# Kernel optimization log

Measured on AMD Instinct MI355X. Metric: run time of the kernel, lower is better.

Reference implementation:

```python
import jax, jax.numpy as jnp
import numpy as np

A_BITS = 7   # activation - 1, per T_quantize(norm(x), activation-1)
W_BITS = 7   # weight quantization levels bits (IRlinear, bit=weight)
HEADS = 16
DIM_HEAD = 64
LN_EPS = 1e-5


def qfn(x, bit):
    """Symmetric per-tensor uniform quantization with straight-through estimator.
    bit >= 31 means bypass (fp path, matching weight/activation == 32 defaults)."""
    if bit >= 31:
        return x
    n = jnp.asarray(2.0 ** bit - 1.0, x.dtype)
    s = jnp.max(jnp.abs(x))
    s = jnp.where(s == 0, jnp.asarray(1.0, x.dtype), s)
    y = jnp.round(x / s * n) / n * s
    # STE: forward uses quantized value, gradient passes through unchanged
    return x + jax.lax.stop_gradient(y - x)


def setup_inputs() -> dict:
    key = jax.random.key(0)
    kx, kq, ko = jax.random.split(key, 3)
    B, N, C = 8, 1024, 1024
    inner = HEADS * DIM_HEAD  # 1024
    x = jax.random.normal(kx, (B, N, C), dtype=jnp.float32)
    gamma = jnp.ones((C,), dtype=jnp.float32)
    beta = jnp.zeros((C,), dtype=jnp.float32)
    W_qkv = jax.random.normal(kq, (3 * inner, C), dtype=jnp.float32) * 0.02
    W_out = jax.random.normal(ko, (C, inner), dtype=jnp.float32) * 0.02
    b_out = jnp.zeros((C,), dtype=jnp.float32)
    return {"x": x, "gamma": gamma, "beta": beta,
            "W_qkv": W_qkv, "W_out": W_out, "b_out": b_out}


def reference(x, gamma, beta, W_qkv, W_out, b_out):
    B, N, C = x.shape
    H, Dh = HEADS, DIM_HEAD
    # LayerNorm
    mu = jnp.mean(x, axis=-1, keepdims=True)
    var = jnp.mean(jnp.square(x - mu), axis=-1, keepdims=True)
    xn = (x - mu) * jax.lax.rsqrt(var + LN_EPS) * gamma + beta
    # activation quantization (T_quantize with activation-1 bits)
    xq = qfn(xn, A_BITS)
    # quantized QKV projection (IRlinear, no bias)
    qkv = jnp.einsum('bnc,oc->bno', xq, qfn(W_qkv, W_BITS))
    qkv = qkv.reshape(B, N, 3, H, Dh).transpose(2, 0, 3, 1, 4)  # [3,B,H,N,Dh]
    q, k, v = qkv[0], qkv[1], qkv[2]
    # scaled dot-product attention (dropout_p = 0)
    scale = Dh ** -0.5
    scores = jnp.einsum('bhqd,bhkd->bhqk', q, k) * scale
    attn = jax.nn.softmax(scores, axis=-1)
    o = jnp.einsum('bhqk,bhkd->bhqd', attn, v)  # [B,H,N,Dh]
    o = o.transpose(0, 2, 1, 3).reshape(B, N, H * Dh)
    # quantized output projection (IRlinear, with bias)
    out = jnp.einsum('bni,ci->bnc', o, qfn(W_out, W_BITS)) + b_out
    return out
```

## Files before the change

### kernel.cpp

```cpp
#include <hip/hip_runtime.h>
#include <hip/hip_bf16.h>
#include <math.h>

typedef unsigned int u32;
typedef unsigned short u16;
using f32x4  = __attribute__((ext_vector_type(4))) float;
using f32x16 = __attribute__((ext_vector_type(16))) float;
using bfrag  = __attribute__((ext_vector_type(8))) short;
using i32x4  = __attribute__((ext_vector_type(4))) int;
union FragU { uint4 u; bfrag f; };
union FragI { uint4 u; i32x4 f; };

#define HEADS 16
#define DH    64
#define NB    8
#define NN    1024
#define NC    1024
#define M_TOT 8192
#define O_QKV 3072
#define KDIM  1024
#define LOG2E 1.44269504088896340736f

static __device__ __forceinline__ u16 f2bf(float f) {
  u32 u = __float_as_uint(f);
  return (u16)((u + 0x7fffu + ((u >> 16) & 1u)) >> 16);
}
static __device__ __forceinline__ float bf2f(u16 h) { return __uint_as_float(((u32)h) << 16); }
static __device__ __forceinline__ u32 pk_bf16(float a, float b) {
  __hip_bfloat162 h = __float22bfloat162_rn(make_float2(a, b));
  u32 r; __builtin_memcpy(&r, &h, 4); return r;
}

static __device__ __forceinline__ float wave_sum(float v) {
#pragma unroll
  for (int off = 32; off > 0; off >>= 1) v += __shfl_xor(v, off, 64);
  return v;
}
static __device__ __forceinline__ float wave_max(float v) {
#pragma unroll
  for (int off = 32; off > 0; off >>= 1) v = fmaxf(v, __shfl_xor(v, off, 64));
  return v;
}

static __device__ __forceinline__ f32x4 mfma16(FragU a, FragU b, f32x4 c) {
  return __builtin_amdgcn_mfma_f32_16x16x32_bf16(a.f, b.f, c, 0, 0, 0);
}
static __device__ __forceinline__ f32x16 mfma32(FragU a, FragU b, f32x16 c) {
  return __builtin_amdgcn_mfma_f32_32x32x16_bf16(a.f, b.f, c, 0, 0, 0);
}
static __device__ __forceinline__ i32x4 mfma16i(FragI a, FragI b, i32x4 c) {
  return __builtin_amdgcn_mfma_i32_16x16x64_i8(a.f, b.f, c, 0, 0, 0);
}

static __device__ __forceinline__ void pl32swap(u32& a, u32& b) {
#if __has_builtin(__builtin_amdgcn_permlane32_swap)
  using u32x2 = __attribute__((ext_vector_type(2))) unsigned int;
  u32x2 r = __builtin_amdgcn_permlane32_swap(a, b, false, false);
  a = r[0]; b = r[1];
#else
  asm volatile("v_permlane32_swap_b32 %0, %1" : "+v"(a), "+v"(b));
#endif
}

template<int P, int BLK>
static __device__ __forceinline__ void stage_rows(const char* g, int row_stride,
                                                  char* ldsb, int t) {
#pragma unroll
  for (int p = 0; p < P; ++p) {
    const int c = p * BLK + t;
    const int row = c >> 3, kc = c & 7;
    const char* gp = g + (size_t)row * row_stride + ((kc ^ (row & 7)) << 4);
    char* lp = ldsb + ((p * BLK + (t & ~63)) << 4);
    __builtin_amdgcn_global_load_lds((const __attribute__((address_space(1))) void*)gp,
                                     (__attribute__((address_space(3))) void*)lp, 16, 0, 0);
  }
}
static __device__ __forceinline__ uint4 ld_chunk(const char* base, int row, int chunk) {
  return *(const uint4*)(base + (((row << 3) + (chunk ^ (row & 7))) << 4));
}

__global__ __launch_bounds__(256) void absmax2_kernel(const float4* __restrict__ wq,
    const float4* __restrict__ wo, float* __restrict__ wqp, float* __restrict__ wop) {
  const float4* p; int n4, bid, nb; float* o;
  if (blockIdx.x < 512) { p = wq; n4 = O_QKV * KDIM / 4; o = wqp + blockIdx.x; bid = blockIdx.x; nb = 512; }
  else                  { p = wo; n4 = NC * KDIM / 4;    o = wop + blockIdx.x - 512; bid = blockIdx.x - 512; nb = 256; }
  float m = 0.f;
  for (int i = bid * 256 + threadIdx.x; i < n4; i += nb * 256) {
    float4 v = p[i];
    m = fmaxf(m, fmaxf(fmaxf(fabsf(v.x), fabsf(v.y)), fmaxf(fabsf(v.z), fabsf(v.w))));
  }
  m = wave_max(m);
  __shared__ float red[4];
  if ((threadIdx.x & 63) == 0) red[threadIdx.x >> 6] = m;
  __syncthreads();
  if (threadIdx.x == 0) *o = fmaxf(fmaxf(red[0], red[1]), fmaxf(red[2], red[3]));
}

__global__ __launch_bounds__(256) void ln_pass(const float* __restrict__ x,
    const float* __restrict__ g, const float* __restrict__ b,
    float2* __restrict__ mrs, float* __restrict__ actp)
{
  const int t = threadIdx.x, w = t >> 6, l = t & 63;
  const int row = (blockIdx.x << 2) + w;
  const float4* xr = (const float4*)(x + (size_t)row * NC);
  float4 v[4];
#pragma unroll
  for (int j = 0; j < 4; ++j) v[j] = xr[l + (j << 6)];

  float s = 0.f;
#pragma unroll
  for (int j = 0; j < 4; ++j) s += (v[j].x + v[j].y) + (v[j].z + v[j].w);
  s = wave_sum(s);
  const float mu = s * (1.0f / NC);

  float ss = 0.f;
#pragma unroll
  for (int j = 0; j < 4; ++j) {
    const float dx = v[j].x - mu, dy = v[j].y - mu, dz = v[j].z - mu, dw = v[j].w - mu;
    ss += (dx * dx + dy * dy) + (dz * dz + dw * dw);
  }
  ss = wave_sum(ss);
  const float rstd = 1.0f / sqrtf(ss * (1.0f / NC) + 1e-5f);
  if (l == 0) mrs[row] = make_float2(mu, rstd);

  float am = 0.f;
#pragma unroll
  for (int j = 0; j < 4; ++j) {
    const float4 gv = ((const float4*)g)[l + (j << 6)];
    const float4 bv = ((const float4*)b)[l + (j << 6)];
    const float yx = (v[j].x - mu) * rstd * gv.x + bv.x;
    const float yy = (v[j].y - mu) * rstd * gv.y + bv.y;
    const float yz = (v[j].z - mu) * rstd * gv.z + bv.z;
    const float yw = (v[j].w - mu) * rstd * gv.w + bv.w;
    am = fmaxf(am, fmaxf(fmaxf(fabsf(yx), fabsf(yy)), fmaxf(fabsf(yz), fabsf(yw))));
  }
  am = wave_max(am);
  __shared__ float red[4];
  if (l == 0) red[w] = am;
  __syncthreads();
  if (t == 0) actp[blockIdx.x] = fmaxf(fmaxf(red[0], red[1]), fmaxf(red[2], red[3]));
}

__global__ __launch_bounds__(256) void reduce3(const float* __restrict__ actp,
    const float* __restrict__ wqp, const float* __restrict__ wop,
    unsigned* __restrict__ scal)
{
  const int t = threadIdx.x;
  float a = 0.f, q = 0.f, o = 0.f;
#pragma unroll
  for (int k = 0; k < 8; ++k) a = fmaxf(a, actp[t + (k << 8)]);
  a = fmaxf(a, 0.f);
  q = fmaxf(wqp[t], wqp[t + 256]);
  o = wop[t];
  a = wave_max(a); q = wave_max(q); o = wave_max(o);
  __shared__ float ra[4], rq[4], ro[4];
  if ((t & 63) == 0) { ra[t >> 6] = a; rq[t >> 6] = q; ro[t >> 6] = o; }
  __syncthreads();
  if (t == 0) {
    a = fmaxf(fmaxf(ra[0], ra[1]), fmaxf(ra[2], ra[3]));
    q = fmaxf(fmaxf(rq[0], rq[1]), fmaxf(rq[2], rq[3]));
    o = fmaxf(fmaxf(ro[0], ro[1]), fmaxf(ro[2], ro[3]));
    scal[0] = __float_as_uint(a == 0.f ? 1.f : a);
    scal[1] = __float_as_uint(q == 0.f ? 1.f : q);
    scal[2] = __float_as_uint(o == 0.f ? 1.f : o);
  }
}

__global__ __launch_bounds__(256) void quant_x_kernel(const float* __restrict__ x,
    const float* __restrict__ g, const float* __restrict__ b,
    const float2* __restrict__ mrs, const unsigned* __restrict__ sb,
    u32* __restrict__ xq)
{
  const int t = threadIdx.x;
  const long long row = blockIdx.x;
  const float2 ms = mrs[row];
  const float s = __uint_as_float(*sb);
  const float4 v = ((const float4*)(x + row * NC))[t];
  const float4 gv = ((const float4*)g)[t];
  const float4 bv = ((const float4*)b)[t];
  float4 y;
  y.x = (v.x - ms.x) * ms.y * gv.x + bv.x;
  y.y = (v.y - ms.x) * ms.y * gv.y + bv.y;
  y.z = (v.z - ms.x) * ms.y * gv.z + bv.z;
  y.w = (v.w - ms.x) * ms.y * gv.w + bv.w;
  const int ia = (int)rintf(y.x / s * 127.0f);
  const int ib = (int)rintf(y.y / s * 127.0f);
  const int ic = (int)rintf(y.z / s * 127.0f);
  const int id = (int)rintf(y.w / s * 127.0f);
  xq[row * 256 + t] = (u32)(ia & 255) | ((u32)(ib & 255) << 8)
                    | ((u32)(ic & 255) << 16) | ((u32)(id & 255) << 24);
}

__global__ __launch_bounds__(256) void quant_w_kernel(const float4* __restrict__ wq,
    u32* __restrict__ oq, const float4* __restrict__ wo, uint2* __restrict__ oo,
    const unsigned* __restrict__ scal) {
  if (blockIdx.x < 768) {
    const float s = __uint_as_float(scal[1]);
    const int base = blockIdx.x << 10;
#pragma unroll
    for (int k = 0; k < 4; ++k) {
      const int i = base + (k << 8) + threadIdx.x;
      float4 v = wq[i];
      const int ia = (int)rintf(v.x / s * 127.0f);
      const int ib = (int)rintf(v.y / s * 127.0f);
      const int ic = (int)rintf(v.z / s * 127.0f);
      const int id = (int)rintf(v.w / s * 127.0f);
      oq[i] = (u32)(ia & 255) | ((u32)(ib & 255) << 8)
            | ((u32)(ic & 255) << 16) | ((u32)(id & 255) << 24);
    }
  } else {
    const float s = __uint_as_float(scal[2]);
    const int base = (blockIdx.x - 768) << 10;
#pragma unroll
    for (int k = 0; k < 4; ++k) {
      const int i = base + (k << 8) + threadIdx.x;
      float4 v = wo[i];
      uint2 o;
      o.x = pk_bf16(rintf(v.x / s * 127.0f), rintf(v.y / s * 127.0f));
      o.y = pk_bf16(rintf(v.z / s * 127.0f), rintf(v.w / s * 127.0f));
      oo[i] = o;
    }
  }
}

__global__ __launch_bounds__(256) void gemm_qkv_mfma(const char* __restrict__ A,
    const char* __restrict__ B, const unsigned* __restrict__ scal,
    u16* __restrict__ qp, u16* __restrict__ kp, u16* __restrict__ vtp)
{
  __shared__ __align__(16) char lds[32768];
  char* As = lds;
  char* Bs = lds + 16384;
  const int t = threadIdx.x, w = t >> 6, l = t & 63;
  const int lg = l >> 4, lc = l & 15;
  const int wm = (w >> 1) << 6, wn = (w & 1) << 6;
  i32x4 acc[4][4];
#pragma unroll
  for (int i = 0; i < 4; ++i)
#pragma unroll
    for (int j = 0; j < 4; ++j) acc[i][j] = 0;

  const char* gA = A + ((size_t)blockIdx.y << 7) * KDIM;
  const char* gB = B + ((size_t)blockIdx.x << 7) * KDIM;

  for (int k0 = 0; k0 < KDIM; k0 += 128) {
    stage_rows<4, 256>(gA + k0, KDIM, As, t);
    stage_rows<4, 256>(gB + k0, KDIM, Bs, t);
    __syncthreads();
#pragma unroll
    for (int ks = 0; ks < 2; ++ks) {
      FragI a[4], b[4];
#pragma unroll
      for (int mf = 0; mf < 4; ++mf) a[mf].u = ld_chunk(As, wm + (mf << 4) + lc, (ks << 2) + lg);
#pragma unroll
      for (int nf = 0; nf < 4; ++nf) b[nf].u = ld_chunk(Bs, wn + (nf << 4) + lc, (ks << 2) + lg);
      __builtin_amdgcn_s_setprio(1);
#pragma unroll
      for (int mf = 0; mf < 4; ++mf)
#pragma unroll
        for (int nf = 0; nf < 4; ++nf) acc[mf][nf] = mfma16i(a[mf], b[nf], acc[mf][nf]);
      __builtin_amdgcn_s_setprio(0);
    }
    __syncthreads();
  }

  const float sa = __uint_as_float(scal[0]), sw = __uint_as_float(scal[1]);
  const int which = blockIdx.x >> 3;
  float sc = sa * sw / 16129.0f;
  if (which == 0) sc *= 0.125f * LOG2E;
  const int obase = ((blockIdx.x & 7) << 7) + wn;
  const int mbase = ((int)blockIdx.y << 7) + wm;

  if (which < 2) {
    u16* d_ = which ? kp : qp;
#pragma unroll
    for (int nf = 0; nf < 4; ++nf) {
      const int od = obase + (nf << 4) + lc;
      const int hh = od >> 6, dd = od & 63;
#pragma unroll
      for (int mf = 0; mf < 4; ++mf)
#pragma unroll
        for (int r = 0; r < 4; ++r) {
          const int tok = mbase + (mf << 4) + (lg << 2) + r;
          const size_t addr = ((size_t)((tok >> 10) * HEADS + hh) << 16)
                            + ((size_t)(tok & 1023) << 6) + dd;
          d_[addr] = f2bf((float)acc[mf][nf][r] * sc);
        }
    }
  } else {
#pragma unroll
    for (int nf = 0; nf < 4; ++nf) {
      const int od = obase + (nf << 4) + lc;
      const int hh = od >> 6, dd = od & 63;
#pragma unroll
      for (int mf = 0; mf < 4; ++mf) {
        const int tok0 = mbase + (mf << 4) + (lg << 2);
        uint2 hv;
        hv.x = pk_bf16((float)acc[mf][nf][0] * sc, (float)acc[mf][nf][1] * sc);
        hv.y = pk_bf16((float)acc[mf][nf][2] * sc, (float)acc[mf][nf][3] * sc);
        const size_t base = ((size_t)((tok0 >> 10) * HEADS + hh) << 16)
                          + ((size_t)dd << 10) + (tok0 & 1023);
        *(uint2*)(vtp + base) = hv;
      }
    }
  }
}

__global__ __launch_bounds__(512) void attn_mfma(
    const u16* __restrict__ qp, const u16* __restrict__ kp, const u16* __restrict__ vtp,
    u16* __restrict__ ohp)
{
  __shared__ __align__(16) char lds[32768];
  const int t = threadIdx.x, w = t >> 6, l = t & 63;
  const int l31 = l & 31, h = l >> 5;
  const int id = blockIdx.x;
  const int bh = ((id & 7) << 4) + ((id >> 3) & 15);
  const int qbase = ((id >> 7) << 8) + (w << 5);
  const size_t bhoff = (size_t)bh << 16;

  FragU qf[4];
#pragma unroll
  for (int ks = 0; ks < 4; ++ks)
    qf[ks].u = *(const uint4*)(qp + bhoff + ((size_t)(qbase + l31) << 6) + (ks << 4) + (h << 3));

  f32x16 oacc[2];
  oacc[0] = 0.f; oacc[1] = 0.f;
  float lpart = 0.f;

  stage_rows<1, 512>((const char*)(kp + bhoff), 128, lds, t);
  stage_rows<1, 512>((const char*)(vtp + bhoff), 2048, lds + 8192, t);
  __syncthreads();

  for (int kb = 0; kb < 16; ++kb) {
    char* cur = lds + ((kb & 1) << 14);
    if (kb < 15) {
      char* nxt = lds + (((kb + 1) & 1) << 14);
      const size_t kn = kb + 1;
      stage_rows<1, 512>((const char*)(kp + bhoff + (kn << 12)), 128, nxt, t);
      stage_rows<1, 512>((const char*)(vtp + bhoff + (kn << 6)), 2048, nxt + 8192, t);
    }

    f32x16 s0 = 0.f, s1 = 0.f;
#pragma unroll
    for (int ks = 0; ks < 4; ++ks) {
      FragU k0, k1;
      k0.u = ld_chunk(cur, l31,      (ks << 1) + h);
      k1.u = ld_chunk(cur, 32 + l31, (ks << 1) + h);
      __builtin_amdgcn_s_setprio(1);
      s0 = mfma32(k0, qf[ks], s0);
      s1 = mfma32(k1, qf[ks], s1);
      __builtin_amdgcn_s_setprio(0);
    }

    u32 W0[8], W1[8];
    float lsum = 0.f;
#pragma unroll
    for (int j = 0; j < 8; ++j) {
      const float a0 = __builtin_amdgcn_exp2f(s0[2 * j]);
      const float b0 = __builtin_amdgcn_exp2f(s0[2 * j + 1]);
      const float a1 = __builtin_amdgcn_exp2f(s1[2 * j]);
      const float b1 = __builtin_amdgcn_exp2f(s1[2 * j + 1]);
      lsum += (a0 + b0) + (a1 + b1);
      W0[j] = pk_bf16(a0, b0);
      W1[j] = pk_bf16(a1, b1);
    }
    lpart += lsum;

    FragU pf[4];
#pragma unroll
    for (int kk = 0; kk < 2; ++kk) {
      u32 a0 = W0[4 * kk + 0], b0 = W0[4 * kk + 2];
      u32 a1 = W0[4 * kk + 1], b1 = W0[4 * kk + 3];
      pl32swap(a0, b0); pl32swap(a1, b1);
      pf[kk].u     = make_uint4(a0, a1, b0, b1);
      u32 c0 = W1[4 * kk + 0], d0 = W1[4 * kk + 2];
      u32 c1 = W1[4 * kk + 1], d1 = W1[4 * kk + 3];
      pl32swap(c0, d0); pl32swap(c1, d1);
      pf[2 + kk].u = make_uint4(c0, c1, d0, d1);
    }

#pragma unroll
    for (int ks = 0; ks < 4; ++ks) {
      FragU v0, v1;
      v0.u = ld_chunk(cur + 8192, l31,      (ks << 1) + h);
      v1.u = ld_chunk(cur + 8192, 32 + l31, (ks << 1) + h);
      __builtin_amdgcn_s_setprio(1);
      oacc[0] = mfma32(v0, pf[ks], oacc[0]);
      oacc[1] = mfma32(v1, pf[ks], oacc[1]);
      __builtin_amdgcn_s_setprio(0);
    }
    __syncthreads();
  }

  lpart += __shfl_xor(lpart, 32, 64);
  const float invl = 1.0f / lpart;

  const int b = bh >> 4, hd_ = bh & 15;
  const size_t orow = (size_t)b * NN + qbase + l31;
  u16* ohb = ohp + (orow << 10) + (hd_ << 6);
#pragma unroll
  for (int dt = 0; dt < 2; ++dt)
#pragma unroll
    for (int rg = 0; rg < 4; ++rg) {
      const int d0 = (dt << 5) + (rg << 3) + (h << 2);
      const float v0 = oacc[dt][4 * rg + 0] * invl, v1 = oacc[dt][4 * rg + 1] * invl;
      const float v2 = oacc[dt][4 * rg + 2] * invl, v3 = oacc[dt][4 * rg + 3] * invl;
      uint2 hv;
      hv.x = (u32)f2bf(v0) | ((u32)f2bf(v1) << 16);
      hv.y = (u32)f2bf(v2) | ((u32)f2bf(v3) << 16);
      *(uint2*)(ohb + d0) = hv;
    }
}

__global__ __launch_bounds__(256) void gemm_out_mfma(const u16* __restrict__ Ah,
    const u16* __restrict__ B, const unsigned* __restrict__ scal,
    const float* __restrict__ bias, float* __restrict__ out)
{
  __shared__ __align__(16) char lds[32768];
  char* Ahs = lds;
  char* Bs  = lds + 16384;
  const int t = threadIdx.x, w = t >> 6, l = t & 63;
  const int lg = l >> 4, lc = l & 15;
  const int wm = (w >> 1) << 6, wn = (w & 1) << 6;
  f32x4 acc[4][4];
#pragma unroll
  for (int i = 0; i < 4; ++i)
#pragma unroll
    for (int j = 0; j < 4; ++j) acc[i][j] = 0.f;

  const char* gAh = (const char*)Ah + ((size_t)blockIdx.y << 7) * 2048;
  const char* gB  = (const char*)B  + ((size_t)blockIdx.x << 7) * 2048;

  for (int k0 = 0; k0 < KDIM; k0 += 64) {
    stage_rows<4, 256>(gAh + k0 * 2, 2048, Ahs, t);
    stage_rows<4, 256>(gB  + k0 * 2, 2048, Bs,  t);
    __syncthreads();
#pragma unroll
    for (int ks = 0; ks < 2; ++ks) {
      FragU a[4], b[4];
#pragma unroll
      for (int mf = 0; mf < 4; ++mf) a[mf].u = ld_chunk(Ahs, wm + (mf << 4) + lc, (ks << 2) + lg);
#pragma unroll
      for (int nf = 0; nf < 4; ++nf) b[nf].u = ld_chunk(Bs, wn + (nf << 4) + lc, (ks << 2) + lg);
      __builtin_amdgcn_s_setprio(1);
#pragma unroll
      for (int mf = 0; mf < 4; ++mf)
#pragma unroll
        for (int nf = 0; nf < 4; ++nf) acc[mf][nf] = mfma16(a[mf], b[nf], acc[mf][nf]);
      __builtin_amdgcn_s_setprio(0);
    }
    __syncthreads();
  }

  const float sc = __uint_as_float(scal[2]) / 127.0f;
  const int cb = ((int)blockIdx.x << 7) + wn;
  const int mb = ((int)blockIdx.y << 7) + wm;
#pragma unroll
  for (int nf = 0; nf < 4; ++nf) {
    const int col = cb + (nf << 4) + lc;
    const float bv = bias[col];
#pragma unroll
    for (int mf = 0; mf < 4; ++mf)
#pragma unroll
      for (int r = 0; r < 4; ++r) {
        const int row = mb + (mf << 4) + (lg << 2) + r;
        out[(size_t)row * NC + col] = acc[mf][nf][r] * sc + bv;
      }
  }
}

__global__ void ws_fail_kernel(float* out) { out[0] = 1.0e6f; }

extern "C" void kernel_launch(void* const* d_in, const int* in_sizes, int n_in,
                              void* d_out, int out_size, void* d_ws, size_t ws_size,
                              hipStream_t stream) {
  const float* x     = (const float*)d_in[0];
  const float* gamma = (const float*)d_in[1];
  const float* beta  = (const float*)d_in[2];
  const float* Wqkv  = (const float*)d_in[3];
  const float* Wout  = (const float*)d_in[4];
  const float* bout  = (const float*)d_in[5];
  float* out = (float*)d_out;

  char* ws = (char*)d_ws;
  unsigned* scal = (unsigned*)ws;
  size_t off = 256;
  float* actp = (float*)(ws + off); off += 2048 * 4;
  float* wqp  = (float*)(ws + off); off += 512 * 4;
  float* wop  = (float*)(ws + off); off += 256 * 4;
  off = (off + 255) & ~(size_t)255;
  float2* mrs = (float2*)(ws + off); off += (size_t)M_TOT * 8;
  char* xq  = ws + off; off += (size_t)M_TOT * KDIM;
  char* wqi = ws + off; off += (size_t)O_QKV * KDIM;
  u16* woi = (u16*)(ws + off); off += (size_t)NC * KDIM * 2;
  u16* qb  = (u16*)(ws + off); off += 16777216;
  u16* kb  = (u16*)(ws + off); off += 16777216;
  u16* vtb = (u16*)(ws + off); off += 16777216;
  u16* oh  = (u16*)(ws + off); off += 16777216;
  if (ws_size < off) { ws_fail_kernel<<<1, 1, 0, stream>>>(out); return; }

  absmax2_kernel<<<768, 256, 0, stream>>>((const float4*)Wqkv, (const float4*)Wout, wqp, wop);
  ln_pass<<<2048, 256, 0, stream>>>(x, gamma, beta, mrs, actp);
  reduce3<<<1, 256, 0, stream>>>(actp, wqp, wop, scal);

  quant_x_kernel<<<M_TOT, 256, 0, stream>>>(x, gamma, beta, mrs, scal + 0, (u32*)xq);
  quant_w_kernel<<<1024, 256, 0, stream>>>((const float4*)Wqkv, (u32*)wqi,
                                           (const float4*)Wout, (uint2*)woi, scal);

  dim3 g1(O_QKV / 128, M_TOT / 128);
  gemm_qkv_mfma<<<g1, 256, 0, stream>>>(xq, wqi, scal, qb, kb, vtb);

  attn_mfma<<<512, 512, 0, stream>>>(qb, kb, vtb, oh);

  dim3 g3(NC / 128, M_TOT / 128);
  gemm_out_mfma<<<g3, 256, 0, stream>>>(oh, woi, scal, bout, out);
}
```

Before: 144.7 us.

## Merge prep kernels and double attention key block to 128

Result: faster. 139.2 us, median of 2 (-3.8%).

```diff
diff --git a/kernel.cpp b/kernel.cpp
--- a/kernel.cpp
+++ b/kernel.cpp
@@ -25,7 +25,6 @@
   u32 u = __float_as_uint(f);
   return (u16)((u + 0x7fffu + ((u >> 16) & 1u)) >> 16);
 }
-static __device__ __forceinline__ float bf2f(u16 h) { return __uint_as_float(((u32)h) << 16); }
 static __device__ __forceinline__ u32 pk_bf16(float a, float b) {
   __hip_bfloat162 h = __float22bfloat162_rn(make_float2(a, b));
   u32 r; __builtin_memcpy(&r, &h, 4); return r;
@@ -79,66 +78,64 @@
   return *(const uint4*)(base + (((row << 3) + (chunk ^ (row & 7))) << 4));
 }
 
-__global__ __launch_bounds__(256) void absmax2_kernel(const float4* __restrict__ wq,
-    const float4* __restrict__ wo, float* __restrict__ wqp, float* __restrict__ wop) {
-  const float4* p; int n4, bid, nb; float* o;
-  if (blockIdx.x < 512) { p = wq; n4 = O_QKV * KDIM / 4; o = wqp + blockIdx.x; bid = blockIdx.x; nb = 512; }
-  else                  { p = wo; n4 = NC * KDIM / 4;    o = wop + blockIdx.x - 512; bid = blockIdx.x - 512; nb = 256; }
-  float m = 0.f;
-  for (int i = bid * 256 + threadIdx.x; i < n4; i += nb * 256) {
-    float4 v = p[i];
-    m = fmaxf(m, fmaxf(fmaxf(fabsf(v.x), fabsf(v.y)), fmaxf(fabsf(v.z), fabsf(v.w))));
-  }
-  m = wave_max(m);
+__global__ __launch_bounds__(256) void prep_kernel(const float* __restrict__ x,
+    const float* __restrict__ g, const float* __restrict__ b,
+    const float4* __restrict__ wq, const float4* __restrict__ wo,
+    float2* __restrict__ mrs, float* __restrict__ actp,
+    float* __restrict__ wqp, float* __restrict__ wop)
+{
   __shared__ float red[4];
-  if ((threadIdx.x & 63) == 0) red[threadIdx.x >> 6] = m;
-  __syncthreads();
-  if (threadIdx.x == 0) *o = fmaxf(fmaxf(red[0], red[1]), fmaxf(red[2], red[3]));
-}
-
-__global__ __launch_bounds__(256) void ln_pass(const float* __restrict__ x,
-    const float* __restrict__ g, const float* __restrict__ b,
-    float2* __restrict__ mrs, float* __restrict__ actp)
-{
-  const int t = threadIdx.x, w = t >> 6, l = t & 63;
-  const int row = (blockIdx.x << 2) + w;
-  const float4* xr = (const float4*)(x + (size_t)row * NC);
-  float4 v[4];
-#pragma unroll
-  for (int j = 0; j < 4; ++j) v[j] = xr[l + (j << 6)];
-
-  float s = 0.f;
-#pragma unroll
-  for (int j = 0; j < 4; ++j) s += (v[j].x + v[j].y) + (v[j].z + v[j].w);
-  s = wave_sum(s);
-  const float mu = s * (1.0f / NC);
-
-  float ss = 0.f;
-#pragma unroll
-  for (int j = 0; j < 4; ++j) {
-    const float dx = v[j].x - mu, dy = v[j].y - mu, dz = v[j].z - mu, dw = v[j].w - mu;
-    ss += (dx * dx + dy * dy) + (dz * dz + dw * dw);
-  }
-  ss = wave_sum(ss);
-  const float rstd = 1.0f / sqrtf(ss * (1.0f / NC) + 1e-5f);
-  if (l == 0) mrs[row] = make_float2(mu, rstd);
-
-  float am = 0.f;
-#pragma unroll
-  for (int j = 0; j < 4; ++j) {
-    const float4 gv = ((const float4*)g)[l + (j << 6)];
-    const float4 bv = ((const float4*)b)[l + (j << 6)];
-    const float yx = (v[j].x - mu) * rstd * gv.x + bv.x;
-    const float yy = (v[j].y - mu) * rstd * gv.y + bv.y;
-    const float yz = (v[j].z - mu) * rstd * gv.z + bv.z;
-    const float yw = (v[j].w - mu) * rstd * gv.w + bv.w;
-    am = fmaxf(am, fmaxf(fmaxf(fabsf(yx), fabsf(yy)), fmaxf(fabsf(yz), fabsf(yw))));
-  }
-  am = wave_max(am);
-  __shared__ float red[4];
-  if (l == 0) red[w] = am;
-  __syncthreads();
-  if (t == 0) actp[blockIdx.x] = fmaxf(fmaxf(red[0], red[1]), fmaxf(red[2], red[3]));
+  const int bid = blockIdx.x, t = threadIdx.x;
+  if (bid < 2048) {
+    const int w = t >> 6, l = t & 63;
+    const int row = (bid << 2) + w;
+    const float4* xr = (const float4*)(x + (size_t)row * NC);
+    float4 v[4];
+#pragma unroll
+    for (int j = 0; j < 4; ++j) v[j] = xr[l + (j << 6)];
+    float s = 0.f;
+#pragma unroll
+    for (int j = 0; j < 4; ++j) s += (v[j].x + v[j].y) + (v[j].z + v[j].w);
+    s = wave_sum(s);
+    const float mu = s * (1.0f / NC);
+    float ss = 0.f;
+#pragma unroll
+    for (int j = 0; j < 4; ++j) {
+      const float dx = v[j].x - mu, dy = v[j].y - mu, dz = v[j].z - mu, dw = v[j].w - mu;
+      ss += (dx * dx + dy * dy) + (dz * dz + dw * dw);
+    }
+    ss = wave_sum(ss);
+    const float rstd = 1.0f / sqrtf(ss * (1.0f / NC) + 1e-5f);
+    if (l == 0) mrs[row] = make_float2(mu, rstd);
+    float am = 0.f;
+#pragma unroll
+    for (int j = 0; j < 4; ++j) {
+      const float4 gv = ((const float4*)g)[l + (j << 6)];
+      const float4 bv = ((const float4*)b)[l + (j << 6)];
+      const float yx = (v[j].x - mu) * rstd * gv.x + bv.x;
+      const float yy = (v[j].y - mu) * rstd * gv.y + bv.y;
+      const float yz = (v[j].z - mu) * rstd * gv.z + bv.z;
+      const float yw = (v[j].w - mu) * rstd * gv.w + bv.w;
+      am = fmaxf(am, fmaxf(fmaxf(fabsf(yx), fabsf(yy)), fmaxf(fabsf(yz), fabsf(yw))));
+    }
+    am = wave_max(am);
+    if (l == 0) red[w] = am;
+    __syncthreads();
+    if (t == 0) actp[bid] = fmaxf(fmaxf(red[0], red[1]), fmaxf(red[2], red[3]));
+  } else {
+    const float4* p; int n4, lb, nb; float* o;
+    if (bid < 2560) { p = wq; n4 = O_QKV * KDIM / 4; lb = bid - 2048; nb = 512; o = wqp + lb; }
+    else            { p = wo; n4 = NC * KDIM / 4;    lb = bid - 2560; nb = 256; o = wop + lb; }
+    float m = 0.f;
+    for (int i = lb * 256 + t; i < n4; i += nb * 256) {
+      float4 v = p[i];
+      m = fmaxf(m, fmaxf(fmaxf(fabsf(v.x), fabsf(v.y)), fmaxf(fabsf(v.z), fabsf(v.w))));
+    }
+    m = wave_max(m);
+    if ((t & 63) == 0) red[t >> 6] = m;
+    __syncthreads();
+    if (t == 0) *o = fmaxf(fmaxf(red[0], red[1]), fmaxf(red[2], red[3]));
+  }
 }
 
 __global__ __launch_bounds__(256) void reduce3(const float* __restrict__ actp,
@@ -149,7 +146,6 @@
   float a = 0.f, q = 0.f, o = 0.f;
 #pragma unroll
   for (int k = 0; k < 8; ++k) a = fmaxf(a, actp[t + (k << 8)]);
-  a = fmaxf(a, 0.f);
   q = fmaxf(wqp[t], wqp[t + 256]);
   o = wop[t];
   a = wave_max(a); q = wave_max(q); o = wave_max(o);
@@ -166,40 +162,37 @@
   }
 }
 
-__global__ __launch_bounds__(256) void quant_x_kernel(const float* __restrict__ x,
+__global__ __launch_bounds__(256) void quant_all(const float* __restrict__ x,
     const float* __restrict__ g, const float* __restrict__ b,
-    const float2* __restrict__ mrs, const unsigned* __restrict__ sb,
-    u32* __restrict__ xq)
+    const float2* __restrict__ mrs, const unsigned* __restrict__ scal,
+    u32* __restrict__ xq, const float4* __restrict__ wq, u32* __restrict__ oq,
+    const float4* __restrict__ wo, uint2* __restrict__ oo)
 {
-  const int t = threadIdx.x;
-  const long long row = blockIdx.x;
-  const float2 ms = mrs[row];
-  const float s = __uint_as_float(*sb);
-  const float4 v = ((const float4*)(x + row * NC))[t];
-  const float4 gv = ((const float4*)g)[t];
-  const float4 bv = ((const float4*)b)[t];
-  float4 y;
-  y.x = (v.x - ms.x) * ms.y * gv.x + bv.x;
-  y.y = (v.y - ms.x) * ms.y * gv.y + bv.y;
-  y.z = (v.z - ms.x) * ms.y * gv.z + bv.z;
-  y.w = (v.w - ms.x) * ms.y * gv.w + bv.w;
-  const int ia = (int)rintf(y.x / s * 127.0f);
-  const int ib = (int)rintf(y.y / s * 127.0f);
-  const int ic = (int)rintf(y.z / s * 127.0f);
-  const int id = (int)rintf(y.w / s * 127.0f);
-  xq[row * 256 + t] = (u32)(ia & 255) | ((u32)(ib & 255) << 8)
-                    | ((u32)(ic & 255) << 16) | ((u32)(id & 255) << 24);
-}
-
-__global__ __launch_bounds__(256) void quant_w_kernel(const float4* __restrict__ wq,
-    u32* __restrict__ oq, const float4* __restrict__ wo, uint2* __restrict__ oo,
-    const unsigned* __restrict__ scal) {
-  if (blockIdx.x < 768) {
+  const int bid = blockIdx.x, t = threadIdx.x;
+  if (bid < 8192) {
+    const long long row = bid;
+    const float2 ms = mrs[row];
+    const float s = __uint_as_float(scal[0]);
+    const float4 v = ((const float4*)(x + row * NC))[t];
+    const float4 gv = ((const float4*)g)[t];
+    const float4 bv = ((const float4*)b)[t];
+    float4 y;
+    y.x = (v.x - ms.x) * ms.y * gv.x + bv.x;
+    y.y = (v.y - ms.x) * ms.y * gv.y + bv.y;
+    y.z = (v.z - ms.x) * ms.y * gv.z + bv.z;
+    y.w = (v.w - ms.x) * ms.y * gv.w + bv.w;
+    const int ia = (int)rintf(y.x / s * 127.0f);
+    const int ib = (int)rintf(y.y / s * 127.0f);
+    const int ic = (int)rintf(y.z / s * 127.0f);
+    const int id = (int)rintf(y.w / s * 127.0f);
+    xq[row * 256 + t] = (u32)(ia & 255) | ((u32)(ib & 255) << 8)
+                      | ((u32)(ic & 255) << 16) | ((u32)(id & 255) << 24);
+  } else if (bid < 8960) {
     const float s = __uint_as_float(scal[1]);
-    const int base = blockIdx.x << 10;
+    const int base = (bid - 8192) << 10;
 #pragma unroll
     for (int k = 0; k < 4; ++k) {
-      const int i = base + (k << 8) + threadIdx.x;
+      const int i = base + (k << 8) + t;
       float4 v = wq[i];
       const int ia = (int)rintf(v.x / s * 127.0f);
       const int ib = (int)rintf(v.y / s * 127.0f);
@@ -210,10 +203,10 @@
     }
   } else {
     const float s = __uint_as_float(scal[2]);
-    const int base = (blockIdx.x - 768) << 10;
+    const int base = (bid - 8960) << 10;
 #pragma unroll
     for (int k = 0; k < 4; ++k) {
-      const int i = base + (k << 8) + threadIdx.x;
+      const int i = base + (k << 8) + t;
       float4 v = wo[i];
       uint2 o;
       o.x = pk_bf16(rintf(v.x / s * 127.0f), rintf(v.y / s * 127.0f));
@@ -309,7 +302,7 @@
     const u16* __restrict__ qp, const u16* __restrict__ kp, const u16* __restrict__ vtp,
     u16* __restrict__ ohp)
 {
-  __shared__ __align__(16) char lds[32768];
+  __shared__ __align__(16) char lds[65536];
   const int t = threadIdx.x, w = t >> 6, l = t & 63;
   const int l31 = l & 31, h = l >> 5;
   const int id = blockIdx.x;
@@ -326,67 +319,64 @@
   oacc[0] = 0.f; oacc[1] = 0.f;
   float lpart = 0.f;
 
-  stage_rows<1, 512>((const char*)(kp + bhoff), 128, lds, t);
-  stage_rows<1, 512>((const char*)(vtp + bhoff), 2048, lds + 8192, t);
+  stage_rows<2, 512>((const char*)(kp + bhoff), 128, lds, t);
+  stage_rows<1, 512>((const char*)(vtp + bhoff), 2048, lds + 16384, t);
+  stage_rows<1, 512>((const char*)(vtp + bhoff + 64), 2048, lds + 24576, t);
   __syncthreads();
 
-  for (int kb = 0; kb < 16; ++kb) {
-    char* cur = lds + ((kb & 1) << 14);
-    if (kb < 15) {
-      char* nxt = lds + (((kb + 1) & 1) << 14);
+  for (int kb = 0; kb < 8; ++kb) {
+    char* cur = lds + ((kb & 1) << 15);
+    if (kb < 7) {
+      char* nxt = lds + (((kb + 1) & 1) << 15);
       const size_t kn = kb + 1;
-      stage_rows<1, 512>((const char*)(kp + bhoff + (kn << 12)), 128, nxt, t);
-      stage_rows<1, 512>((const char*)(vtp + bhoff + (kn << 6)), 2048, nxt + 8192, t);
-    }
-
-    f32x16 s0 = 0.f, s1 = 0.f;
-#pragma unroll
-    for (int ks = 0; ks < 4; ++ks) {
-      FragU k0, k1;
-      k0.u = ld_chunk(cur, l31,      (ks << 1) + h);
-      k1.u = ld_chunk(cur, 32 + l31, (ks << 1) + h);
-      __builtin_amdgcn_s_setprio(1);
-      s0 = mfma32(k0, qf[ks], s0);
-      s1 = mfma32(k1, qf[ks], s1);
-      __builtin_amdgcn_s_setprio(0);
-    }
-
-    u32 W0[8], W1[8];
-    float lsum = 0.f;
-#pragma unroll
-    for (int j = 0; j < 8; ++j) {
-      const float a0 = __builtin_amdgcn_exp2f(s0[2 * j]);
-      const float b0 = __builtin_amdgcn_exp2f(s0[2 * j + 1]);
-      const float a1 = __builtin_amdgcn_exp2f(s1[2 * j]);
-      const float b1 = __builtin_amdgcn_exp2f(s1[2 * j + 1]);
-      lsum += (a0 + b0) + (a1 + b1);
-      W0[j] = pk_bf16(a0, b0);
-      W1[j] = pk_bf16(a1, b1);
-    }
-    lpart += lsum;
-
-    FragU pf[4];
-#pragma unroll
-    for (int kk = 0; kk < 2; ++kk) {
-      u32 a0 = W0[4 * kk + 0], b0 = W0[4 * kk + 2];
-      u32 a1 = W0[4 * kk + 1], b1 = W0[4 * kk + 3];
-      pl32swap(a0, b0); pl32swap(a1, b1);
-      pf[kk].u     = make_uint4(a0, a1, b0, b1);
-      u32 c0 = W1[4 * kk + 0], d0 = W1[4 * kk + 2];
-      u32 c1 = W1[4 * kk + 1], d1 = W1[4 * kk + 3];
-      pl32swap(c0, d0); pl32swap(c1, d1);
-      pf[2 + kk].u = make_uint4(c0, c1, d0, d1);
-    }
-
-#pragma unroll
-    for (int ks = 0; ks < 4; ++ks) {
-      FragU v0, v1;
-      v0.u = ld_chunk(cur + 8192, l31,      (ks << 1) + h);
-      v1.u = ld_chunk(cur + 8192, 32 + l31, (ks << 1) + h);
-      __builtin_amdgcn_s_setprio(1);
-      oacc[0] = mfma32(v0, pf[ks], oacc[0]);
-      oacc[1] = mfma32(v1, pf[ks], oacc[1]);
-      __builtin_amdgcn_s_setprio(0);
+      stage_rows<2, 512>((const char*)(kp + bhoff + (kn << 13)), 128, nxt, t);
+      stage_rows<1, 512>((const char*)(vtp + bhoff + (kn << 7)), 2048, nxt + 16384, t);
+      stage_rows<1, 512>((const char*)(vtp + bhoff + (kn << 7) + 64), 2048, nxt + 24576, t);
+    }
+
+#pragma unroll
+    for (int sub = 0; sub < 4; ++sub) {
+      f32x16 s = 0.f;
+#pragma unroll
+      for (int ks = 0; ks < 4; ++ks) {
+        FragU kf;
+        kf.u = ld_chunk(cur, (sub << 5) + l31, (ks << 1) + h);
+        __builtin_amdgcn_s_setprio(1);
+        s = mfma32(kf, qf[ks], s);
+        __builtin_amdgcn_s_setprio(0);
+      }
+
+      u32 W[8];
+      float lsum = 0.f;
+#pragma unroll
+      for (int j = 0; j < 8; ++j) {
+        const float a = __builtin_amdgcn_exp2f(s[2 * j]);
+        const float b = __builtin_amdgcn_exp2f(s[2 * j + 1]);
+        lsum += a + b;
+        W[j] = pk_bf16(a, b);
+      }
+      lpart += lsum;
+
+      FragU pf[2];
+#pragma unroll
+      for (int kk = 0; kk < 2; ++kk) {
+        u32 a0 = W[4 * kk + 0], b0 = W[4 * kk + 2];
+        u32 a1 = W[4 * kk + 1], b1 = W[4 * kk + 3];
+        pl32swap(a0, b0); pl32swap(a1, b1);
+        pf[kk].u = make_uint4(a0, a1, b0, b1);
+      }
+
+      char* Vh = cur + 16384 + ((sub >> 1) << 13);
+#pragma unroll
+      for (int ks = 0; ks < 2; ++ks)
+#pragma unroll
+        for (int dt = 0; dt < 2; ++dt) {
+          FragU vf;
+          vf.u = ld_chunk(Vh, (dt << 5) + l31, ((sub & 1) << 2) + (ks << 1) + h);
+          __builtin_amdgcn_s_setprio(1);
+          oacc[dt] = mfma32(vf, pf[ks], oacc[dt]);
+          __builtin_amdgcn_s_setprio(0);
+        }
     }
     __syncthreads();
   }
@@ -498,13 +488,12 @@
   u16* oh  = (u16*)(ws + off); off += 16777216;
   if (ws_size < off) { ws_fail_kernel<<<1, 1, 0, stream>>>(out); return; }
 
-  absmax2_kernel<<<768, 256, 0, stream>>>((const float4*)Wqkv, (const float4*)Wout, wqp, wop);
-  ln_pass<<<2048, 256, 0, stream>>>(x, gamma, beta, mrs, actp);
+  prep_kernel<<<2816, 256, 0, stream>>>(x, gamma, beta, (const float4*)Wqkv,
+                                        (const float4*)Wout, mrs, actp, wqp, wop);
   reduce3<<<1, 256, 0, stream>>>(actp, wqp, wop, scal);
-
-  quant_x_kernel<<<M_TOT, 256, 0, stream>>>(x, gamma, beta, mrs, scal + 0, (u32*)xq);
-  quant_w_kernel<<<1024, 256, 0, stream>>>((const float4*)Wqkv, (u32*)wqi,
-                                           (const float4*)Wout, (uint2*)woi, scal);
+  quant_all<<<9216, 256, 0, stream>>>(x, gamma, beta, mrs, scal, (u32*)xq,
+                                      (const float4*)Wqkv, (u32*)wqi,
+                                      (const float4*)Wout, (uint2*)woi);
 
   dim3 g1(O_QKV / 128, M_TOT / 128);
   gemm_qkv_mfma<<<g1, 256, 0, stream>>>(xq, wqi, scal, qb, kb, vtb);
```
